# Kernel tuning notes

Measured on AMD Instinct MI355X. Metric: run time of the kernel, lower is better.

## Reference

```python
import jax, jax.numpy as jnp
import numpy as np

SEQ, BATCH = 512, 32
VOCAB, HID, FF = 32000, 1024, 4096
HEADS, NX, MAXLEN = 8, 6, 512
EPS = 1e-5


def _full_layer_norm(t):
    # F.layer_norm(t, t.shape): normalize over ALL elements, no affine
    m = jnp.mean(t)
    v = jnp.mean((t - m) ** 2)
    return (t - m) * jax.lax.rsqrt(v + EPS)


def _attention(x, wq, bq, wk, bk, wv, bv, wo, bo):
    # x: [S, B, H]; faithful to the module's quirky reshape:
    # view(B, S//heads, heads, H) splits the SEQUENCE dim across heads,
    # each head keeps the full feature dim H; scores scaled by sqrt(H//heads).
    S, B, H = x.shape
    head_dim = H // HEADS
    q = x @ wq + bq
    k = x @ wk + bk
    v = x @ wv + bv

    def split(t):  # [S,B,H] -> [B, heads, S//heads, H]
        return t.transpose(1, 0, 2).reshape(B, S // HEADS, HEADS, H).transpose(0, 2, 1, 3)

    qh, kh, vh = split(q), split(k), split(v)
    energy = jnp.einsum('bhtf,bhsf->bhts', qh, kh) / np.sqrt(head_dim)
    att = jax.nn.softmax(energy, axis=-1)          # [B, heads, S//h, S//h]
    va = jnp.einsum('bhts,bhsf->bhtf', att, vh)    # [B, heads, S//h, H]
    va = va.transpose(2, 0, 1, 3).reshape(S, B, H)  # back to [S, B, H]
    return va @ wo + bo


def _sub_encoder(x, p, i):
    a = _attention(x, p['wq'][i], p['bq'][i], p['wk'][i], p['bk'][i],
                   p['wv'][i], p['bv'][i], p['wo'][i], p['bo'][i])
    mid = _full_layer_norm(a + x)
    f = jax.nn.relu(mid @ p['w1'][i] + p['b1'][i]) @ p['w2'][i] + p['b2'][i]
    return _full_layer_norm(mid + f)


def setup_inputs() -> dict:
    key = jax.random.key(0)
    ks = jax.random.split(key, 16)
    s = 0.02
    inp = {
        'x': jax.random.randint(ks[0], (SEQ, BATCH), 0, VOCAB),
        'emb': jax.random.normal(ks[1], (VOCAB, HID), jnp.float32) * s,
        'pos_emb': jax.random.normal(ks[2], (MAXLEN, HID), jnp.float32) * s,
        'wq': jax.random.normal(ks[3], (NX, HID, HID), jnp.float32) * s,
        'bq': jnp.zeros((NX, HID), jnp.float32),
        'wk': jax.random.normal(ks[4], (NX, HID, HID), jnp.float32) * s,
        'bk': jnp.zeros((NX, HID), jnp.float32),
        'wv': jax.random.normal(ks[5], (NX, HID, HID), jnp.float32) * s,
        'bv': jnp.zeros((NX, HID), jnp.float32),
        'wo': jax.random.normal(ks[6], (NX, HID, HID), jnp.float32) * s,
        'bo': jnp.zeros((NX, HID), jnp.float32),
        'w1': jax.random.normal(ks[7], (NX, HID, FF), jnp.float32) * s,
        'b1': jnp.zeros((NX, FF), jnp.float32),
        'w2': jax.random.normal(ks[8], (NX, FF, HID), jnp.float32) * s,
        'b2': jnp.zeros((NX, HID), jnp.float32),
    }
    return inp


def reference(x, emb, pos_emb, wq, bq, wk, bk, wv, bv, wo, bo, w1, b1, w2, b2):
    # dropout layers are identity (eval mode); src_mask=None path
    S = x.shape[0]
    p = dict(wq=wq, bq=bq, wk=wk, bk=bk, wv=wv, bv=bv, wo=wo, bo=bo,
             w1=w1, b1=b1, w2=w2, b2=b2)
    h = emb[x] * np.sqrt(HID) + pos_emb[jnp.arange(S)][:, None, :]
    for i in range(NX):
        h = _sub_encoder(h, p, i)
    return h
```

## Files before the change

### kernel.cpp

```cpp
#include <hip/hip_runtime.h>
#include <hip/hip_bf16.h>
#include <stdint.h>

typedef __bf16 bf16_t;
typedef __bf16 bf16x8 __attribute__((ext_vector_type(8)));
typedef __bf16 bf16x4 __attribute__((ext_vector_type(4)));
typedef float  f32x16 __attribute__((ext_vector_type(16)));

#define SEQ   512
#define BATCH 32
#define HID   1024
#define FFD   4096
#define NROW  (SEQ*BATCH)
#define NTOT  ((long)NROW*HID)
#define QKVS  3072

typedef __attribute__((address_space(3))) uint32_t lds_u32;
typedef __attribute__((address_space(1))) const uint32_t glb_u32;

__device__ __forceinline__ void gload_lds16(const void* g, void* l) {
  glb_u32* gp = reinterpret_cast<glb_u32*>(reinterpret_cast<uintptr_t>(g));
  lds_u32* lp = reinterpret_cast<lds_u32*>(reinterpret_cast<uintptr_t>(l));
  __builtin_amdgcn_global_load_lds(gp, lp, 16, 0, 0);
}

__global__ __launch_bounds__(256) void embed_k(const int* __restrict__ x,
    const float* __restrict__ emb, const float* __restrict__ pos,
    bf16_t* __restrict__ hb, float* __restrict__ stId)
{
  if (blockIdx.x == 0 && threadIdx.x == 0) { stId[0] = 0.f; stId[1] = 1.f; }
  const long row = blockIdx.x;
  const int  s   = (int)(row >> 5);
  const long idx = x[row];
  const int  t   = threadIdx.x;
  float4 e  = ((const float4*)(emb + idx*HID))[t];
  float4 pv = ((const float4*)(pos + (long)s*HID))[t];
  bf16x4 ob = {(bf16_t)(e.x*32.f+pv.x), (bf16_t)(e.y*32.f+pv.y),
               (bf16_t)(e.z*32.f+pv.z), (bf16_t)(e.w*32.f+pv.w)};
  *(bf16x4*)(hb + row*HID + (long)t*4) = ob;
}

__device__ __forceinline__ void wcvtNL_body(const float* __restrict__ W,
    bf16_t* __restrict__ wT, int K, int N, int bid)
{
  const int t  = threadIdx.x;
  const int nt = N >> 9;
  const int n  = ((bid % nt) << 9) + t;
  const int k0 = (bid / nt) << 6;
#pragma unroll
  for (int kb = 0; kb < 64; kb += 8) {
    bf16x8 o;
#pragma unroll
    for (int j = 0; j < 8; ++j)
      o[j] = (bf16_t)W[(long)(k0 + kb + j)*N + n];
    *(bf16x8*)&wT[(long)n*K + k0 + kb] = o;
  }
}

__device__ __forceinline__ void csum512_body(const float* __restrict__ W,
    float* __restrict__ out, int K, int N, int bid)
{
  const int n = bid*512 + threadIdx.x;
  float s0 = 0.f, s1 = 0.f, s2 = 0.f, s3 = 0.f;
  for (int k = 0; k < K; k += 4) {
    s0 += W[(long)k*N + n];
    s1 += W[(long)(k+1)*N + n];
    s2 += W[(long)(k+2)*N + n];
    s3 += W[(long)(k+3)*N + n];
  }
  out[n] = (s0 + s1) + (s2 + s3);
}

__global__ __launch_bounds__(512) void prep0(const float* __restrict__ wq,
    const float* __restrict__ wk, const float* __restrict__ wv,
    bf16_t* __restrict__ wT3, float* __restrict__ cs3)
{
  const int b = blockIdx.x;
  if (b < 96) {
    const int sel = b >> 5;
    const float* W = sel == 0 ? wq : sel == 1 ? wk : wv;
    wcvtNL_body(W, wT3 + (size_t)sel*HID*HID, HID, HID, b & 31);
  } else {
    const int col = (b - 96)*512 + threadIdx.x;
    const int sel = col >> 10, n = col & 1023;
    const float* W = sel == 0 ? wq : sel == 1 ? wk : wv;
    float s = 0.f;
    for (int k = 0; k < HID; ++k) s += W[(long)k*HID + n];
    cs3[col] = s;
  }
}

__global__ __launch_bounds__(512) void prep_k(
    const float* __restrict__ Wo, bf16_t* __restrict__ wTo,
    const float* __restrict__ W1, bf16_t* __restrict__ wT1, float* __restrict__ cs1,
    const float* __restrict__ W2, bf16_t* __restrict__ wT2,
    const float* __restrict__ Wq, const float* __restrict__ Wk,
    const float* __restrict__ Wv, bf16_t* __restrict__ wT3,
    float* __restrict__ cs3)
{
  const int b = blockIdx.x;
  if (b < 32)        wcvtNL_body(Wo, wTo, HID, HID, b);
  else if (b < 160)  wcvtNL_body(W1, wT1, HID, FFD, b - 32);
  else if (b < 288)  wcvtNL_body(W2, wT2, FFD, HID, b - 160);
  else if (b < 296)  csum512_body(W1, cs1, HID, FFD, b - 288);
  else if (b < 392) {
    const int i = b - 296, sel = i >> 5;
    const float* W = sel == 0 ? Wq : sel == 1 ? Wk : Wv;
    wcvtNL_body(W, wT3 + (size_t)sel*HID*HID, HID, HID, i & 31);
  } else {
    const int col = (b - 392)*512 + threadIdx.x;
    const int sel = col >> 10, n = col & 1023;
    const float* W = sel == 0 ? Wq : sel == 1 ? Wk : Wv;
    float s = 0.f;
    for (int k = 0; k < HID; ++k) s += W[(long)k*HID + n];
    cs3[col] = s;
  }
}

template<int MODE>
__global__ __launch_bounds__(512, 4)
void gemmW(const bf16_t* __restrict__ A, const bf16_t* __restrict__ Bt,
           const float* __restrict__ ba, const float* __restrict__ bb,
           const float* __restrict__ bc, const float* __restrict__ cs,
           const float* __restrict__ stats, const bf16_t* __restrict__ res,
           bf16_t* __restrict__ outB, float* __restrict__ part,
           int M, int N, int K)
{
  __shared__ bf16_t As[128][64];
  __shared__ bf16_t Bs[256][64];
  __shared__ float  rs[512], rq[512];
  const int tid = threadIdx.x;
  const int w = tid >> 6, l = tid & 63;
  const int wm = w >> 2, wn = w & 3;
  const int lr = l & 31, hi = l >> 5;

  const int nbn = N >> 8;
  const int nwg = gridDim.x;
  const int q8 = nwg >> 3, r8 = nwg & 7;
  const int xcd = blockIdx.x & 7, bidx = blockIdx.x >> 3;
  const int wg = (xcd < r8 ? xcd*(q8+1) : r8*(q8+1) + (xcd-r8)*q8) + bidx;
  const long bm = wg / nbn, bn = wg % nbn;
  const long rA0 = bm << 7, rB0 = bn << 8;

  const int srow   = tid >> 3;
  const int schunk = (((tid & 7) ^ ((tid >> 3) & 7)) << 3);
  const int ldsw   = (tid >> 6) << 10;

  f32x16 a00 = {0}, a01 = {0}, a10 = {0}, a11 = {0};

#define STG_TILE(kt) do { \
    const long kb_ = (long)(kt)*64 + schunk; \
    gload_lds16(A  + (rA0 + srow)*(long)K + kb_,        (char*)As + ldsw); \
    gload_lds16(A  + (rA0 + 64 + srow)*(long)K + kb_,   (char*)As + 8192 + ldsw); \
    gload_lds16(Bt + (rB0 + srow)*(long)K + kb_,        (char*)Bs + ldsw); \
    gload_lds16(Bt + (rB0 + 64 + srow)*(long)K + kb_,   (char*)Bs + 8192 + ldsw); \
    gload_lds16(Bt + (rB0 + 128 + srow)*(long)K + kb_,  (char*)Bs + 16384 + ldsw); \
    gload_lds16(Bt + (rB0 + 192 + srow)*(long)K + kb_,  (char*)Bs + 24576 + ldsw); \
  } while (0)
#define FRA(mt, kk) (*(const bf16x8*)((const char*)As + (wm*64 + (mt)*32 + lr)*128 + \
                      ((((kk)*2 + hi) ^ (l & 7)) << 4)))
#define FRB(nt, kk) (*(const bf16x8*)((const char*)Bs + (wn*64 + (nt)*32 + lr)*128 + \
                      ((((kk)*2 + hi) ^ (l & 7)) << 4)))

  const int nk = K >> 6;
  for (int t = 0; t < nk; ++t) {
    __syncthreads();
    STG_TILE(t);
    __syncthreads();
#pragma unroll
    for (int kk = 0; kk < 4; ++kk) {
      bf16x8 fa0 = FRA(0, kk), fa1 = FRA(1, kk);
      bf16x8 fb0 = FRB(0, kk), fb1 = FRB(1, kk);
      a00 = __builtin_amdgcn_mfma_f32_32x32x16_bf16(fa0, fb0, a00, 0, 0, 0);
      a01 = __builtin_amdgcn_mfma_f32_32x32x16_bf16(fa0, fb1, a01, 0, 0, 0);
      a10 = __builtin_amdgcn_mfma_f32_32x32x16_bf16(fa1, fb0, a10, 0, 0, 0);
      a11 = __builtin_amdgcn_mfma_f32_32x32x16_bf16(fa1, fb1, a11, 0, 0, 0);
    }
  }
#undef STG_TILE
#undef FRA
#undef FRB

  const float mS = stats[0], rS = stats[1];
  const bool q3 = (N == 3072);
  float ls = 0.f, lsq = 0.f;
  const long rowT = rA0 + wm*64 + 4*hi;
  const long colT = rB0 + wn*64 + lr;
#pragma unroll
  for (int nt = 0; nt < 2; ++nt) {
    const long col = colT + nt*32;
    float bv;
    if (MODE == 3 && q3)
      bv = col < 1024 ? ba[col] : col < 2048 ? bb[col - 1024] : bc[col - 2048];
    else
      bv = ba[col];
    float beta = 0.f;
    if (MODE == 3 || MODE == 4) beta = bv - mS*rS*cs[col];
#pragma unroll
    for (int mt = 0; mt < 2; ++mt) {
      const f32x16 acc = mt == 0 ? (nt == 0 ? a00 : a01) : (nt == 0 ? a10 : a11);
#pragma unroll
      for (int r = 0; r < 16; ++r) {
        const long row = rowT + mt*32 + (r & 3) + 8*(r >> 2);
        const long off = row*(long)N + col;
        float v;
        if (MODE == 3)      v = fmaf(acc[r], rS, beta);
        else if (MODE == 4) v = fmaxf(fmaf(acc[r], rS, beta), 0.f);
        else {
          v = acc[r] + bv + ((float)res[off] - mS)*rS;
          ls += v; lsq += v*v;
        }
        outB[off] = (bf16_t)v;
      }
    }
  }
  if (MODE == 5) {
    rs[tid] = ls; rq[tid] = lsq;
    __syncthreads();
    for (int o = 256; o > 0; o >>= 1) {
      if (tid < o) { rs[tid] += rs[tid+o]; rq[tid] += rq[tid+o]; }
      __syncthreads();
    }
    if (tid == 0) { part[2*blockIdx.x] = rs[0]; part[2*blockIdx.x + 1] = rq[0]; }
  }
}

__global__ __launch_bounds__(512) void attn_k(
    const bf16_t* __restrict__ qkv, bf16_t* __restrict__ ob)
{
  __shared__ __align__(16) char smem[64*128*2*2 + 64*64*4 + 64*4];
  bf16_t* Qc = (bf16_t*)smem;
  bf16_t* Kc = (bf16_t*)(smem + 16384);
  bf16_t* Vc = (bf16_t*)smem;
  float*  E    = (float*)(smem + 32768);
  float*  Rinv = (float*)(smem + 49152);

  const int tid  = threadIdx.x;
  const int head = blockIdx.x & 7, b = blockIdx.x >> 3;
  const long rbase = (long)head*32 + b;

  const int ti = tid >> 3, g = tid & 7;
  const int lr = tid >> 3;

  float eacc[8];
#pragma unroll
  for (int j = 0; j < 8; ++j) eacc[j] = 0.f;

  for (int kc = 0; kc < HID; kc += 128) {
    __syncthreads();
    const bf16_t* qrow = qkv + (lr*256 + rbase)*QKVS + kc;
    const bf16_t* krow = qkv + (lr*256 + rbase)*QKVS + 1024 + kc;
#pragma unroll
    for (int i = 0; i < 2; ++i) {
      const int p = i*8 + g;
      const int src = (p ^ (lr & 7)) * 8;
      *(uint4*)&Qc[lr*128 + p*8] = *(const uint4*)&qrow[src];
      *(uint4*)&Kc[lr*128 + p*8] = *(const uint4*)&krow[src];
    }
    __syncthreads();
    for (int e8 = 0; e8 < 16; ++e8) {
      const int qp = e8 ^ (ti & 7);
      bf16x8 qv = *(bf16x8*)&Qc[ti*128 + qp*8];
      float qf[8];
#pragma unroll
      for (int u = 0; u < 8; ++u) qf[u] = (float)qv[u];
#pragma unroll
      for (int j = 0; j < 8; ++j) {
        const int s  = j*8 + g;
        const int kp = e8 ^ (s & 7);
        bf16x8 kv = *(bf16x8*)&Kc[s*128 + kp*8];
        float a = eacc[j];
#pragma unroll
        for (int u = 0; u < 8; ++u) a += qf[u] * (float)kv[u];
        eacc[j] = a;
      }
    }
  }
  const float scale = 0.0883883476483184f;
  float mx = -1e30f;
#pragma unroll
  for (int j = 0; j < 8; ++j) { eacc[j] *= scale; mx = fmaxf(mx, eacc[j]); }
  mx = fmaxf(mx, __shfl_xor(mx, 1));
  mx = fmaxf(mx, __shfl_xor(mx, 2));
  mx = fmaxf(mx, __shfl_xor(mx, 4));
  float sum = 0.f;
#pragma unroll
  for (int j = 0; j < 8; ++j) {
    const float pj = __expf(eacc[j] - mx);
    const int s = j*8 + g;
    E[s*64 + (ti ^ (s & 7))] = pj;
    sum += pj;
  }
  sum += __shfl_xor(sum, 1);
  sum += __shfl_xor(sum, 2);
  sum += __shfl_xor(sum, 4);
  if (g == 0) Rinv[ti] = 1.f / sum;
  __syncthreads();

  const int lane = tid & 63, w8 = tid >> 6;
  const float rv = Rinv[lane];
  const long orow = (long)lane*256 + b*8 + head;
  for (int fc = 0; fc < HID; fc += 128) {
    __syncthreads();
    const bf16_t* vrow = qkv + (lr*256 + rbase)*QKVS + 2048 + fc;
#pragma unroll
    for (int i = 0; i < 2; ++i) {
      const int p = i*8 + g;
      *(uint4*)&Vc[lr*128 + p*8] = *(const uint4*)&vrow[p*8];
    }
    __syncthreads();
    float vacc[16];
#pragma unroll
    for (int u = 0; u < 16; ++u) vacc[u] = 0.f;
    for (int s = 0; s < 64; ++s) {
      const float pp = E[s*64 + (lane ^ (s & 7))];
#pragma unroll
      for (int u = 0; u < 2; ++u) {
        bf16x8 vv = *(bf16x8*)&Vc[s*128 + w8*16 + u*8];
#pragma unroll
        for (int t8 = 0; t8 < 8; ++t8) vacc[u*8 + t8] += pp * (float)vv[t8];
      }
    }
#pragma unroll
    for (int u = 0; u < 2; ++u) {
      bf16x8 ov;
#pragma unroll
      for (int t8 = 0; t8 < 8; ++t8) ov[t8] = (bf16_t)(vacc[u*8 + t8] * rv);
      *(bf16x8*)&ob[orow*HID + fc + w8*16 + u*8] = ov;
    }
  }
}

__global__ __launch_bounds__(256) void reduce2(const float* __restrict__ part,
                                               float* __restrict__ stats, int np)
{
  __shared__ double sh[256], sh2[256];
  const int tid = threadIdx.x;
  double s = 0.0, s2 = 0.0;
  for (int i = tid; i < np; i += 256) { s += part[2*i]; s2 += part[2*i + 1]; }
  sh[tid] = s; sh2[tid] = s2; __syncthreads();
  for (int o = 128; o > 0; o >>= 1) {
    if (tid < o) { sh[tid] += sh[tid+o]; sh2[tid] += sh2[tid+o]; }
    __syncthreads();
  }
  if (tid == 0) {
    const double n = (double)NTOT;
    const double mean = sh[0] / n;
    const double var  = sh2[0] / n - mean*mean;
    stats[0] = (float)mean;
    stats[1] = (float)(1.0 / sqrt(var + 1e-5));
  }
}

__global__ __launch_bounds__(256) void final_norm(const bf16_t* __restrict__ t,
    const float* __restrict__ stats, float* __restrict__ out)
{
  const float m = stats[0], r = stats[1];
  const long n8 = NTOT / 8;
  for (long i = (long)blockIdx.x*blockDim.x + threadIdx.x; i < n8;
       i += (long)gridDim.x*blockDim.x) {
    bf16x8 v = ((const bf16x8*)t)[i];
    float4 o0 = {((float)v[0]-m)*r, ((float)v[1]-m)*r, ((float)v[2]-m)*r, ((float)v[3]-m)*r};
    float4 o1 = {((float)v[4]-m)*r, ((float)v[5]-m)*r, ((float)v[6]-m)*r, ((float)v[7]-m)*r};
    ((float4*)out)[2*i]   = o0;
    ((float4*)out)[2*i+1] = o1;
  }
}

extern "C" void kernel_launch(void* const* d_in, const int* in_sizes, int n_in,
                              void* d_out, int out_size, void* d_ws, size_t ws_size,
                              hipStream_t stream)
{
  const int*   x    = (const int*)  d_in[0];
  const float* emb  = (const float*)d_in[1];
  const float* pos  = (const float*)d_in[2];
  const float* wq_a = (const float*)d_in[3];
  const float* bq_a = (const float*)d_in[4];
  const float* wk_a = (const float*)d_in[5];
  const float* bk_a = (const float*)d_in[6];
  const float* wv_a = (const float*)d_in[7];
  const float* bv_a = (const float*)d_in[8];
  const float* wo_a = (const float*)d_in[9];
  const float* bo_a = (const float*)d_in[10];
  const float* w1_a = (const float*)d_in[11];
  const float* b1_a = (const float*)d_in[12];
  const float* w2_a = (const float*)d_in[13];
  const float* b2_a = (const float*)d_in[14];

  char* p = (char*)d_ws;
  auto take = [&](size_t n) { char* r = p; p += (n + 255) & ~(size_t)255; return r; };
  bf16_t* hb   = (bf16_t*)take(NTOT*2);
  bf16_t* U    = (bf16_t*)take((size_t)NROW*FFD*2);
  bf16_t* qkv  = U;
  bf16_t* attb = U + 3*NTOT;
  bf16_t* ffb  = U;
  bf16_t* wTo  = (bf16_t*)take((size_t)HID*HID*2);
  bf16_t* wT1  = (bf16_t*)take((size_t)HID*FFD*2);
  bf16_t* wT2  = (bf16_t*)take((size_t)HID*FFD*2);
  bf16_t* wT3  = (bf16_t*)take((size_t)3*HID*HID*2);
  float*  cs1  = (float*) take(FFD*4);
  float*  cs3  = (float*) take(QKVS*4);
  float*  part = (float*) take(4096*4);
  float*  stId = (float*) take(256);
  float*  st1  = (float*) take(256);
  float*  st2  = (float*) take(256);

  const int gQKV = (NROW/128)*(QKVS/256);
  const int gH   = (NROW/128)*(HID/256);
  const int gF   = (NROW/128)*(FFD/256);

  embed_k<<<NROW, 256, 0, stream>>>(x, emb, pos, hb, stId);
  prep0<<<102, 512, 0, stream>>>(wq_a, wk_a, wv_a, wT3, cs3);

  for (int i = 0; i < 6; ++i) {
    const float* Bq = bq_a + (size_t)i*HID;
    const float* Bk = bk_a + (size_t)i*HID;
    const float* Bv = bv_a + (size_t)i*HID;
    const float* Wo = wo_a + (size_t)i*HID*HID;  const float* Bo = bo_a + (size_t)i*HID;
    const float* W1 = w1_a + (size_t)i*HID*FFD;  const float* B1 = b1_a + (size_t)i*FFD;
    const float* W2 = w2_a + (size_t)i*FFD*HID;  const float* B2 = b2_a + (size_t)i*HID;
    const float* stIn = (i == 0) ? stId : st2;
    const int haveNext = (i < 5);
    const float* Wqn = wq_a + (size_t)(i+1)*HID*HID;
    const float* Wkn = wk_a + (size_t)(i+1)*HID*HID;
    const float* Wvn = wv_a + (size_t)(i+1)*HID*HID;

    gemmW<3><<<gQKV, 512, 0, stream>>>(hb, wT3, Bq, Bk, Bv, cs3, stIn,
                                       nullptr, qkv, nullptr, NROW, QKVS, HID);

    attn_k<<<256, 512, 0, stream>>>(qkv, attb);

    prep_k<<<haveNext ? 398 : 296, 512, 0, stream>>>(
        Wo, wTo, W1, wT1, cs1, W2, wT2, Wqn, Wkn, Wvn, wT3, cs3);

    gemmW<5><<<gH, 512, 0, stream>>>(attb, wTo, Bo, Bo, Bo, nullptr, stIn,
                                     hb, hb, part, NROW, HID, HID);
    reduce2<<<1, 256, 0, stream>>>(part, st1, gH);

    gemmW<4><<<gF, 512, 0, stream>>>(hb, wT1, B1, B1, B1, cs1, st1,
                                     nullptr, ffb, nullptr, NROW, FFD, HID);

    gemmW<5><<<gH, 512, 0, stream>>>(ffb, wT2, B2, B2, B2, nullptr, st1,
                                     hb, hb, part, NROW, HID, FFD);
    reduce2<<<1, 256, 0, stream>>>(part, st2, gH);
  }

  final_norm<<<2048, 256, 0, stream>>>(hb, st2, (float*)d_out);
}
```

Baseline: 4.054 ms.

## Rewrite attention kernel with MFMA bf16 matrix ops and async LDS loads

Replaces the scalar-FMA attention kernel with one that computes QK^T and PV using 16x16x32 bf16 MFMA instructions, four waves per block instead of eight. Q/K tiles are loaded with direct global-to-LDS loads, softmax probabilities are stored as bf16 in LDS, V is transposed into LDS, and outputs are staged through LDS for coalesced stores. This targets the scalar arithmetic cost of the attention step; it adds rounding of probabilities to bf16 and extra LDS transposes and barriers.

```diff
diff --git a/kernel.cpp b/kernel.cpp
--- a/kernel.cpp
+++ b/kernel.cpp
@@ -5,6 +5,7 @@
 typedef __bf16 bf16_t;
 typedef __bf16 bf16x8 __attribute__((ext_vector_type(8)));
 typedef __bf16 bf16x4 __attribute__((ext_vector_type(4)));
+typedef float  f32x4  __attribute__((ext_vector_type(4)));
 typedef float  f32x16 __attribute__((ext_vector_type(16)));
 
 #define SEQ   512
@@ -225,108 +226,120 @@
   }
 }
 
-__global__ __launch_bounds__(512) void attn_k(
+__global__ __launch_bounds__(256) void attn_m(
     const bf16_t* __restrict__ qkv, bf16_t* __restrict__ ob)
 {
-  __shared__ __align__(16) char smem[64*128*2*2 + 64*64*4 + 64*4];
-  bf16_t* Qc = (bf16_t*)smem;
-  bf16_t* Kc = (bf16_t*)(smem + 16384);
-  bf16_t* Vc = (bf16_t*)smem;
-  float*  E    = (float*)(smem + 32768);
-  float*  Rinv = (float*)(smem + 49152);
-
-  const int tid  = threadIdx.x;
+  __shared__ __align__(16) bf16_t QK[2][8192];
+  __shared__ __align__(16) bf16_t Ps[64*64];
+  bf16_t* Vs = &QK[0][0];
+  bf16_t* Os = &QK[1][0];
+
+  const int tid = threadIdx.x;
+  const int w = tid >> 6, l = tid & 63;
+  const int fr = l & 15, kq = l >> 4;
   const int head = blockIdx.x & 7, b = blockIdx.x >> 3;
   const long rbase = (long)head*32 + b;
 
-  const int ti = tid >> 3, g = tid & 7;
-  const int lr = tid >> 3;
-
-  float eacc[8];
-#pragma unroll
-  for (int j = 0; j < 8; ++j) eacc[j] = 0.f;
+  const int lr  = tid >> 2;
+  const int sslot = (tid & 15) ^ (tid >> 4);
+
+  f32x4 accS[4] = {{0,0,0,0},{0,0,0,0},{0,0,0,0},{0,0,0,0}};
 
   for (int kc = 0; kc < HID; kc += 128) {
     __syncthreads();
-    const bf16_t* qrow = qkv + (lr*256 + rbase)*QKVS + kc;
-    const bf16_t* krow = qkv + (lr*256 + rbase)*QKVS + 1024 + kc;
-#pragma unroll
-    for (int i = 0; i < 2; ++i) {
-      const int p = i*8 + g;
-      const int src = (p ^ (lr & 7)) * 8;
-      *(uint4*)&Qc[lr*128 + p*8] = *(const uint4*)&qrow[src];
-      *(uint4*)&Kc[lr*128 + p*8] = *(const uint4*)&krow[src];
-    }
-    __syncthreads();
-    for (int e8 = 0; e8 < 16; ++e8) {
-      const int qp = e8 ^ (ti & 7);
-      bf16x8 qv = *(bf16x8*)&Qc[ti*128 + qp*8];
-      float qf[8];
-#pragma unroll
-      for (int u = 0; u < 8; ++u) qf[u] = (float)qv[u];
+#pragma unroll
+    for (int i = 0; i < 4; ++i) {
+      const int r = i*16 + (tid >> 4);
+      const long gq = ((long)r*256 + rbase)*QKVS + kc + sslot*8;
+      gload_lds16(qkv + gq,        (char*)&QK[0][0] + i*4096 + w*1024);
+      gload_lds16(qkv + gq + 1024, (char*)&QK[1][0] + i*4096 + w*1024);
+    }
+    __syncthreads();
+#pragma unroll
+    for (int kk = 0; kk < 4; ++kk) {
+      const int ra = w*16 + fr;
+      bf16x8 a = *(const bf16x8*)&QK[0][ra*128 + (((kk*4 + kq) ^ fr) << 3)];
+#pragma unroll
+      for (int n = 0; n < 4; ++n) {
+        const int rb = n*16 + fr;
+        bf16x8 bv = *(const bf16x8*)&QK[1][rb*128 + (((kk*4 + kq) ^ fr) << 3)];
+        accS[n] = __builtin_amdgcn_mfma_f32_16x16x32_bf16(a, bv, accS[n], 0, 0, 0);
+      }
+    }
+  }
+
+  const float scale = 0.08838834764831843f;
+  float pj[4][4];
+#pragma unroll
+  for (int j = 0; j < 4; ++j) {
+    float m = fmaxf(fmaxf(accS[0][j], accS[1][j]), fmaxf(accS[2][j], accS[3][j]));
+    m = fmaxf(m, __shfl_xor(m, 1));
+    m = fmaxf(m, __shfl_xor(m, 2));
+    m = fmaxf(m, __shfl_xor(m, 4));
+    m = fmaxf(m, __shfl_xor(m, 8));
+    m *= scale;
+    float s = 0.f;
+#pragma unroll
+    for (int n = 0; n < 4; ++n) { pj[n][j] = __expf(accS[n][j]*scale - m); s += pj[n][j]; }
+    s += __shfl_xor(s, 1);
+    s += __shfl_xor(s, 2);
+    s += __shfl_xor(s, 4);
+    s += __shfl_xor(s, 8);
+    const float rv = 1.f / s;
+#pragma unroll
+    for (int n = 0; n < 4; ++n) pj[n][j] *= rv;
+  }
+#pragma unroll
+  for (int n = 0; n < 4; ++n)
+#pragma unroll
+    for (int j = 0; j < 4; ++j) {
+      const int r = w*16 + kq*4 + j;
+      const int cpos = n*16 + fr;
+      Ps[r*64 + (((cpos >> 3) ^ (r & 7)) << 3) + (cpos & 7)] = (bf16_t)pj[n][j];
+    }
+  __syncthreads();
+
+  const long orow = (long)lr*256 + b*8 + head;
+  for (int fc = 0; fc < HID; fc += 128) {
+    const bf16_t* vrow = qkv + ((long)lr*256 + rbase)*QKVS + 2048 + fc;
+#pragma unroll
+    for (int i = 0; i < 4; ++i) {
+      const int f0 = (tid & 3)*8 + i*32;
+      uint4 vv = *(const uint4*)&vrow[f0];
+      const bf16_t* ve = (const bf16_t*)&vv;
 #pragma unroll
       for (int j = 0; j < 8; ++j) {
-        const int s  = j*8 + g;
-        const int kp = e8 ^ (s & 7);
-        bf16x8 kv = *(bf16x8*)&Kc[s*128 + kp*8];
-        float a = eacc[j];
-#pragma unroll
-        for (int u = 0; u < 8; ++u) a += qf[u] * (float)kv[u];
-        eacc[j] = a;
+        const int f = f0 + j;
+        Vs[f*64 + (((lr >> 3) ^ (f & 7)) << 3) + (lr & 7)] = ve[j];
       }
     }
-  }
-  const float scale = 0.0883883476483184f;
-  float mx = -1e30f;
-#pragma unroll
-  for (int j = 0; j < 8; ++j) { eacc[j] *= scale; mx = fmaxf(mx, eacc[j]); }
-  mx = fmaxf(mx, __shfl_xor(mx, 1));
-  mx = fmaxf(mx, __shfl_xor(mx, 2));
-  mx = fmaxf(mx, __shfl_xor(mx, 4));
-  float sum = 0.f;
-#pragma unroll
-  for (int j = 0; j < 8; ++j) {
-    const float pj = __expf(eacc[j] - mx);
-    const int s = j*8 + g;
-    E[s*64 + (ti ^ (s & 7))] = pj;
-    sum += pj;
-  }
-  sum += __shfl_xor(sum, 1);
-  sum += __shfl_xor(sum, 2);
-  sum += __shfl_xor(sum, 4);
-  if (g == 0) Rinv[ti] = 1.f / sum;
-  __syncthreads();
-
-  const int lane = tid & 63, w8 = tid >> 6;
-  const float rv = Rinv[lane];
-  const long orow = (long)lane*256 + b*8 + head;
-  for (int fc = 0; fc < HID; fc += 128) {
-    __syncthreads();
-    const bf16_t* vrow = qkv + (lr*256 + rbase)*QKVS + 2048 + fc;
-#pragma unroll
-    for (int i = 0; i < 2; ++i) {
-      const int p = i*8 + g;
-      *(uint4*)&Vc[lr*128 + p*8] = *(const uint4*)&vrow[p*8];
-    }
-    __syncthreads();
-    float vacc[16];
-#pragma unroll
-    for (int u = 0; u < 16; ++u) vacc[u] = 0.f;
-    for (int s = 0; s < 64; ++s) {
-      const float pp = E[s*64 + (lane ^ (s & 7))];
-#pragma unroll
-      for (int u = 0; u < 2; ++u) {
-        bf16x8 vv = *(bf16x8*)&Vc[s*128 + w8*16 + u*8];
-#pragma unroll
-        for (int t8 = 0; t8 < 8; ++t8) vacc[u*8 + t8] += pp * (float)vv[t8];
+    __syncthreads();
+    const int ra = w*16 + fr;
+    bf16x8 a0 = *(const bf16x8*)&Ps[ra*64 + ((kq       ^ (ra & 7)) << 3)];
+    bf16x8 a1 = *(const bf16x8*)&Ps[ra*64 + (((4 + kq) ^ (ra & 7)) << 3)];
+    f32x4 accO[8];
+#pragma unroll
+    for (int nt = 0; nt < 8; ++nt) {
+      const int f = nt*16 + fr;
+      bf16x8 b0 = *(const bf16x8*)&Vs[f*64 + ((kq       ^ (f & 7)) << 3)];
+      bf16x8 b1 = *(const bf16x8*)&Vs[f*64 + (((4 + kq) ^ (f & 7)) << 3)];
+      accO[nt] = __builtin_amdgcn_mfma_f32_16x16x32_bf16(a0, b0, (f32x4){0.f,0.f,0.f,0.f}, 0, 0, 0);
+      accO[nt] = __builtin_amdgcn_mfma_f32_16x16x32_bf16(a1, b1, accO[nt], 0, 0, 0);
+    }
+#pragma unroll
+    for (int nt = 0; nt < 8; ++nt)
+#pragma unroll
+      for (int j = 0; j < 4; ++j) {
+        const int r = w*16 + kq*4 + j;
+        const int cpos = nt*16 + fr;
+        Os[r*128 + (((cpos >> 3) ^ (r & 7)) << 3) + (cpos & 7)] = (bf16_t)accO[nt][j];
       }
-    }
-#pragma unroll
-    for (int u = 0; u < 2; ++u) {
-      bf16x8 ov;
-#pragma unroll
-      for (int t8 = 0; t8 < 8; ++t8) ov[t8] = (bf16_t)(vacc[u*8 + t8] * rv);
-      *(bf16x8*)&ob[orow*HID + fc + w8*16 + u*8] = ov;
+    __syncthreads();
+#pragma unroll
+    for (int i = 0; i < 4; ++i) {
+      const int p = (tid & 3)*4 + i;
+      uint4 vv = *(const uint4*)&Os[lr*128 + ((p ^ (lr & 7)) << 3)];
+      *(uint4*)&ob[orow*HID + fc + p*8] = vv;
     }
   }
 }
@@ -428,7 +441,7 @@
     gemmW<3><<<gQKV, 512, 0, stream>>>(hb, wT3, Bq, Bk, Bv, cs3, stIn,
                                        nullptr, qkv, nullptr, NROW, QKVS, HID);
 
-    attn_k<<<256, 512, 0, stream>>>(qkv, attb);
+    attn_m<<<256, 256, 0, stream>>>(qkv, attb);
 
     prep_k<<<haveNext ? 398 : 296, 512, 0, stream>>>(
         Wo, wTo, W1, wT1, cs1, W2, wT2, Wqn, Wkn, Wvn, wT3, cs3);
```

New measurement: 3.452 ms. 1.17x faster.
